# Kernel tuning notes

Hardware: AMD Instinct MI355X
Metric: run time of the kernel (lower is better)

## Reference

```python
import jax, jax.numpy as jnp
import numpy as np
import itertools

N_BOX = 19
B = 2048
T = 5
_EDGES = np.array(list(itertools.combinations(range(N_BOX), 2)))  # [E,2], E=171
ROW = jnp.asarray(_EDGES[:, 0])
COL = jnp.asarray(_EDGES[:, 1])


def setup_inputs() -> dict:
    key = jax.random.key(0)
    ks = jax.random.split(key, 8)
    return {
        "location_t": jax.random.uniform(ks[0], (B, N_BOX, 5), dtype=jnp.float32),
        "feature_t": jax.random.normal(ks[1], (B, N_BOX, 512), dtype=jnp.float32),
        "mask_t": jax.random.randint(ks[2], (B, N_BOX), 0, 2).astype(bool),
        "past_location_t": jax.random.uniform(ks[3], (B, T, N_BOX, 6), dtype=jnp.float32),
        "W1": jax.random.normal(ks[4], (512, 256), dtype=jnp.float32) * 0.05,
        "b1": jax.random.normal(ks[5], (256,), dtype=jnp.float32) * 0.05,
        "W2": jax.random.normal(ks[6], (256, 512), dtype=jnp.float32) * 0.05,
        "b2": jax.random.normal(ks[7], (512,), dtype=jnp.float32) * 0.05,
    }


def _edge_weights(location_t, mask, past_location_t):
    # bbox centers from cols 1..4: [B,N]
    cx = 0.5 * (location_t[:, :, 1] + location_t[:, :, 3])
    cy = 0.5 * (location_t[:, :, 2] + location_t[:, :, 4])
    d = (cx[:, ROW] - cx[:, COL]) ** 2 + (cy[:, ROW] - cy[:, COL]) ** 2  # [B,E]

    # motion distance, vectorized over all nodes then gathered per edge
    cp = past_location_t[:, :, :, 3:-1] - past_location_t[:, :, :, 1:3]  # [B,T,N,2]
    cpx = cp[..., 0] * 1280.0  # [B,T,N]
    cpy = cp[..., 1] * 720.0
    dx = cpx[:, -1] - cpx[:, 0]  # [B,N]
    dy = cpy[:, -1] - cpy[:, 0]
    length = jnp.sqrt(dx ** 2 + dy ** 2)
    length = jnp.where(length == 0.0, 1.0, length)
    ndx = dx / length
    ndy = dy / length
    x0 = cpx[:, 0]  # [B,N]
    y0 = cpy[:, 0]
    d1 = jnp.sqrt((x0[:, ROW] + ndx[:, ROW] - x0[:, COL] - ndx[:, COL]) ** 2
                  + (y0[:, ROW] + ndy[:, ROW] - y0[:, COL] - ndy[:, COL]) ** 2)
    d2 = jnp.sqrt((x0[:, ROW] - x0[:, COL]) ** 2 + (y0[:, ROW] - y0[:, COL]) ** 2)
    md = d1 - d2  # [B,E]

    w = jnp.exp(-(0.7 * d + 0.3 * md))
    valid = mask[:, ROW] & mask[:, COL]
    w = jnp.where(valid, w, 0.0)
    wmin = jnp.min(w, axis=1, keepdims=True)
    wmax = jnp.max(w, axis=1, keepdims=True)
    return (w - wmin) / (wmax - wmin)


def _gcn(x, ew, W, b):
    # PyG GCNConv: add self loops (weight 1), symmetric normalization, x@W, scatter-add, +bias
    n = x.shape[0]
    loops = jnp.arange(n)
    row = jnp.concatenate([ROW, loops])
    col = jnp.concatenate([COL, loops])
    ew_full = jnp.concatenate([ew, jnp.ones((n,), ew.dtype)])
    deg = jax.ops.segment_sum(ew_full, col, num_segments=n)
    dinv = jnp.where(deg > 0, deg ** -0.5, 0.0)
    norm = dinv[row] * ew_full * dinv[col]  # [E+N]
    xw = x @ W  # [N,F_out]
    out = jnp.zeros((n, W.shape[1]), xw.dtype).at[col].add(norm[:, None] * xw[row])
    return out + b


def reference(location_t, feature_t, mask_t, past_location_t, W1, b1, W2, b2):
    w = _edge_weights(location_t, mask_t, past_location_t)  # [B,E]

    def per_graph(x, ew):
        h = jax.nn.sigmoid(_gcn(x, ew, W1, b1))
        return jax.nn.sigmoid(_gcn(h, ew, W2, b2))

    return jax.vmap(per_graph)(feature_t, w)  # [B,19,512]
```

## Files before the change

### kernel.cpp

```cpp
#include <hip/hip_runtime.h>
#include <hip/hip_bf16.h>
#include <math.h>

#define NBOX 19
#define NEDGE 171
#define TT 5
#define BATCH 2048
#define GB 2
#define MR (GB * NBOX)
#define MP 48

typedef __attribute__((ext_vector_type(8))) short short8v;
typedef __attribute__((ext_vector_type(4))) float f32x4;

static __device__ __forceinline__ ushort f2bf(float f) {
    unsigned int u = __builtin_bit_cast(unsigned int, f);
    return (ushort)((u + 0x8000u) >> 16);
}

static __device__ __forceinline__ float sigm(float x) {
    return __builtin_amdgcn_rcpf(1.0f + __expf(-x));
}

__device__ __forceinline__ int edge_index(int r, int c) {
    return r * (NBOX - 1) - (r * (r - 1)) / 2 + (c - r - 1);
}

__global__ __launch_bounds__(192) void adjbf_kernel(
    const float* __restrict__ loc,
    const int*   __restrict__ mask,
    const float* __restrict__ past,
    ushort* __restrict__ adjbf)
{
    int b = blockIdx.x;
    int tid = threadIdx.x;
    __shared__ float cx[NBOX], cy[NBOX], x0[NBOX], y0[NBOX], ndx[NBOX], ndy[NBOX];
    __shared__ int   mv[NBOX];
    __shared__ float w[NEDGE];
    __shared__ float dinv[NBOX];
    __shared__ float wmin_s, wmax_s;

    if (tid < NBOX) {
        const float* l = loc + ((size_t)b * NBOX + tid) * 5;
        cx[tid] = 0.5f * (l[1] + l[3]);
        cy[tid] = 0.5f * (l[2] + l[4]);
        const float* p0 = past + (((size_t)b * TT + 0) * NBOX + tid) * 6;
        const float* p4 = past + (((size_t)b * TT + (TT - 1)) * NBOX + tid) * 6;
        float cpx0 = (p0[3] - p0[1]) * 1280.0f, cpy0 = (p0[4] - p0[2]) * 720.0f;
        float cpx4 = (p4[3] - p4[1]) * 1280.0f, cpy4 = (p4[4] - p4[2]) * 720.0f;
        float dx = cpx4 - cpx0, dy = cpy4 - cpy0;
        float len = sqrtf(dx * dx + dy * dy);
        if (len == 0.0f) len = 1.0f;
        ndx[tid] = dx / len;
        ndy[tid] = dy / len;
        x0[tid] = cpx0;
        y0[tid] = cpy0;
        mv[tid] = mask[(size_t)b * NBOX + tid];
    }
    __syncthreads();

    float wv = 0.0f;
    if (tid < NEDGE) {
        int rem = tid, rr = 0;
        while (rem >= NBOX - 1 - rr) { rem -= NBOX - 1 - rr; rr++; }
        int r = rr, c = rr + 1 + rem;
        float ddx = cx[r] - cx[c], ddy = cy[r] - cy[c];
        float d = ddx * ddx + ddy * ddy;
        float ax = x0[r] + ndx[r] - x0[c] - ndx[c];
        float ay = y0[r] + ndy[r] - y0[c] - ndy[c];
        float d1 = sqrtf(ax * ax + ay * ay);
        float bx = x0[r] - x0[c], by = y0[r] - y0[c];
        float d2 = sqrtf(bx * bx + by * by);
        float md = d1 - d2;
        wv = expf(-(0.7f * d + 0.3f * md));
        if (!(mv[r] && mv[c])) wv = 0.0f;
        w[tid] = wv;
    }
    __syncthreads();

    if (tid == 0) {
        float mn = w[0], mx = w[0];
        for (int i = 1; i < NEDGE; i++) { mn = fminf(mn, w[i]); mx = fmaxf(mx, w[i]); }
        wmin_s = mn; wmax_s = mx;
    }
    __syncthreads();

    float inv_range = 1.0f / (wmax_s - wmin_s);
    if (tid < NEDGE) w[tid] = (wv - wmin_s) * inv_range;
    __syncthreads();

    if (tid < NBOX) {
        float s = 1.0f;
        for (int rr = 0; rr < tid; rr++) s += w[edge_index(rr, tid)];
        dinv[tid] = 1.0f / sqrtf(s);
    }
    __syncthreads();

    ushort* A = adjbf + (size_t)b * 1024;
    for (int idx = tid; idx < 1024; idx += 192) {
        int r = idx & 31, cc = idx >> 5;
        float v = 0.0f;
        if (r < NBOX && cc < NBOX) {
            if (r == cc) v = dinv[r] * dinv[r];
            else if (r < cc) v = w[edge_index(r, cc)] * dinv[r] * dinv[cc];
        }
        A[idx] = f2bf(v);
    }
}

__global__ void packT_kernel(const float* __restrict__ src, ushort* __restrict__ dst,
                             int K, int N)
{
    int total = K * N;
    for (int idx = blockIdx.x * blockDim.x + threadIdx.x; idx < total;
         idx += gridDim.x * blockDim.x) {
        int n = idx / K, k = idx % K;
        dst[idx] = f2bf(src[(size_t)k * N + n]);
    }
}

__global__ __launch_bounds__(256, 4) void fused_kernel(
    const float*  __restrict__ feat,
    const ushort* __restrict__ adjbf,
    const ushort* __restrict__ W1T,
    const ushort* __restrict__ W2T,
    const float*  __restrict__ b1,
    const float*  __restrict__ b2,
    float* __restrict__ out)
{
    __shared__ __align__(16) ushort XHs[MP * 256];
    __shared__ __align__(16) ushort YsT[64 * 64];
    __shared__ __align__(16) ushort AdjS[MP * 64];

    const int tid = threadIdx.x;
    const int lane = tid & 63, wvi = tid >> 6;
    const int rowbase = blockIdx.x * MR;
    const int bbase = blockIdx.x * GB;
    const int ncol = wvi * 16 + (lane & 15);
    const int kgrp = lane >> 4;
    const int l15 = lane & 15;

#pragma unroll
    for (int p = 0; p < 2; p++)
        ((int4*)YsT)[tid + p * 256] = make_int4(0, 0, 0, 0);

    for (int i = tid; i < MP * 64; i += 256) {
        int row = i >> 6, col = i & 63;
        ushort v = 0;
        if (row < MR) {
            int g = (row >= NBOX) ? 1 : 0;
            int cc = row - g * NBOX;
            int rc = col - g * NBOX;
            if ((unsigned)rc < (unsigned)NBOX)
                v = adjbf[(size_t)(bbase + g) * 1024 + cc * 32 + rc];
        }
        int boff = (row * 128 + col * 2) ^ ((row & 7) << 4);
        *(ushort*)((char*)AdjS + boff) = v;
    }

    f32x4 acc1[4][3];
#pragma unroll
    for (int c = 0; c < 4; c++)
#pragma unroll
        for (int m = 0; m < 3; m++) acc1[c][m] = (f32x4){0.f, 0.f, 0.f, 0.f};

    for (int kh = 0; kh < 2; kh++) {
        __syncthreads();
        const float* fg = feat + (size_t)rowbase * 512 + kh * 256;
#pragma unroll
        for (int p = 0; p < 12; p++) {
            int i = tid + p * 256;
            int row = i >> 6, q = i & 63;
            ushort4 h;
            if (i < MR * 64) {
                float4 v = *(const float4*)(fg + (size_t)row * 512 + q * 4);
                h.x = f2bf(v.x); h.y = f2bf(v.y); h.z = f2bf(v.z); h.w = f2bf(v.w);
            } else {
                h.x = 0; h.y = 0; h.z = 0; h.w = 0;
            }
            int boff = (row * 512 + q * 8) ^ ((row & 7) << 4);
            *(ushort4*)((char*)XHs + boff) = h;
        }
        __syncthreads();

        const ushort* bpb = W1T + (size_t)ncol * 512 + kh * 256 + kgrp * 8;
        short8v br[3][4];
#pragma unroll
        for (int c = 0; c < 4; c++)
            br[0][c] = *(const short8v*)(bpb + (size_t)c * 64 * 512);
#pragma unroll
        for (int c = 0; c < 4; c++)
            br[1][c] = *(const short8v*)(bpb + (size_t)c * 64 * 512 + 32);
#pragma unroll
        for (int ks = 0; ks < 8; ks++) {
            if (ks < 6) {
#pragma unroll
                for (int c = 0; c < 4; c++)
                    br[(ks + 2) % 3][c] =
                        *(const short8v*)(bpb + (size_t)c * 64 * 512 + (ks + 2) * 32);
            }
            short8v a[3];
#pragma unroll
            for (int m = 0; m < 3; m++) {
                int row = m * 16 + l15;
                int boff = (row * 512 + ks * 64 + kgrp * 16) ^ ((row & 7) << 4);
                a[m] = *(const short8v*)((char*)XHs + boff);
            }
#pragma unroll
            for (int c = 0; c < 4; c++)
#pragma unroll
                for (int m = 0; m < 3; m++)
                    acc1[c][m] = __builtin_amdgcn_mfma_f32_16x16x32_bf16(
                        a[m], br[ks % 3][c], acc1[c][m], 0, 0, 0);
        }
    }
    __syncthreads();

#pragma unroll
    for (int c = 0; c < 4; c++) {
#pragma unroll
        for (int m = 0; m < 3; m++) {
            int gr0 = m * 16 + kgrp * 4;
            ushort4 hq;
            hq.x = f2bf(acc1[c][m][0]); hq.y = f2bf(acc1[c][m][1]);
            hq.z = f2bf(acc1[c][m][2]); hq.w = f2bf(acc1[c][m][3]);
            int boff = (ncol * 128 + gr0 * 2) ^ ((ncol & 7) << 4);
            *(ushort4*)((char*)YsT + boff) = hq;
        }
        short8v yb[2];
#pragma unroll
        for (int ks = 0; ks < 2; ks++)
            yb[ks] = *(const short8v*)((char*)YsT +
                     ((ncol * 128 + ks * 64 + kgrp * 16) ^ ((ncol & 7) << 4)));
        float bv = b1[c * 64 + ncol];
#pragma unroll
        for (int mt = 0; mt < 3; mt++) {
            f32x4 o = (f32x4){0.f, 0.f, 0.f, 0.f};
#pragma unroll
            for (int ks = 0; ks < 2; ks++) {
                int ar = mt * 16 + l15;
                short8v af = *(const short8v*)((char*)AdjS +
                             ((ar * 128 + ks * 64 + kgrp * 16) ^ ((ar & 7) << 4)));
                o = __builtin_amdgcn_mfma_f32_16x16x32_bf16(af, yb[ks], o, 0, 0, 0);
            }
#pragma unroll
            for (int j = 0; j < 4; j++) {
                int grp = mt * 16 + kgrp * 4 + j;
                float s = sigm(o[j] + bv);
                int boff = (grp * 512 + (c * 64 + ncol) * 2) ^ ((grp & 7) << 4);
                *(ushort*)((char*)XHs + boff) = f2bf(s);
            }
        }
    }
    __syncthreads();

#pragma unroll 1
    for (int half = 0; half < 2; half++) {
        f32x4 acc[4][3];
#pragma unroll
        for (int c = 0; c < 4; c++)
#pragma unroll
            for (int m = 0; m < 3; m++) acc[c][m] = (f32x4){0.f, 0.f, 0.f, 0.f};

        const ushort* bpb = W2T + (size_t)(half * 256 + ncol) * 256 + kgrp * 8;
        short8v br[3][4];
#pragma unroll
        for (int c = 0; c < 4; c++)
            br[0][c] = *(const short8v*)(bpb + (size_t)c * 64 * 256);
#pragma unroll
        for (int c = 0; c < 4; c++)
            br[1][c] = *(const short8v*)(bpb + (size_t)c * 64 * 256 + 32);
#pragma unroll
        for (int ks = 0; ks < 8; ks++) {
            if (ks < 6) {
#pragma unroll
                for (int c = 0; c < 4; c++)
                    br[(ks + 2) % 3][c] =
                        *(const short8v*)(bpb + (size_t)c * 64 * 256 + (ks + 2) * 32);
            }
            short8v a[3];
#pragma unroll
            for (int m = 0; m < 3; m++) {
                int row = m * 16 + l15;
                int boff = (row * 512 + ks * 64 + kgrp * 16) ^ ((row & 7) << 4);
                a[m] = *(const short8v*)((char*)XHs + boff);
            }
#pragma unroll
            for (int c = 0; c < 4; c++)
#pragma unroll
                for (int m = 0; m < 3; m++)
                    acc[c][m] = __builtin_amdgcn_mfma_f32_16x16x32_bf16(
                        a[m], br[ks % 3][c], acc[c][m], 0, 0, 0);
        }

#pragma unroll
        for (int c = 0; c < 4; c++) {
            int cg = half * 4 + c;
#pragma unroll
            for (int m = 0; m < 3; m++) {
                int gr0 = m * 16 + kgrp * 4;
                ushort4 hq;
                hq.x = f2bf(acc[c][m][0]); hq.y = f2bf(acc[c][m][1]);
                hq.z = f2bf(acc[c][m][2]); hq.w = f2bf(acc[c][m][3]);
                int boff = (ncol * 128 + gr0 * 2) ^ ((ncol & 7) << 4);
                *(ushort4*)((char*)YsT + boff) = hq;
            }
            short8v yb[2];
#pragma unroll
            for (int ks = 0; ks < 2; ks++)
                yb[ks] = *(const short8v*)((char*)YsT +
                         ((ncol * 128 + ks * 64 + kgrp * 16) ^ ((ncol & 7) << 4)));
            float bv = b2[cg * 64 + ncol];
#pragma unroll
            for (int mt = 0; mt < 3; mt++) {
                f32x4 o = (f32x4){0.f, 0.f, 0.f, 0.f};
#pragma unroll
                for (int ks = 0; ks < 2; ks++) {
                    int ar = mt * 16 + l15;
                    short8v af = *(const short8v*)((char*)AdjS +
                                 ((ar * 128 + ks * 64 + kgrp * 16) ^ ((ar & 7) << 4)));
                    o = __builtin_amdgcn_mfma_f32_16x16x32_bf16(af, yb[ks], o, 0, 0, 0);
                }
#pragma unroll
                for (int j = 0; j < 4; j++) {
                    int grp = mt * 16 + kgrp * 4 + j;
                    if (grp < MR) {
                        float s = sigm(o[j] + bv);
                        out[(size_t)(rowbase + grp) * 512 + cg * 64 + ncol] = s;
                    }
                }
            }
        }
    }
}

extern "C" void kernel_launch(void* const* d_in, const int* in_sizes, int n_in,
                              void* d_out, int out_size, void* d_ws, size_t ws_size,
                              hipStream_t stream) {
    const float* loc  = (const float*)d_in[0];
    const float* feat = (const float*)d_in[1];
    const int*   mask = (const int*)d_in[2];
    const float* past = (const float*)d_in[3];
    const float* W1   = (const float*)d_in[4];
    const float* b1   = (const float*)d_in[5];
    const float* W2   = (const float*)d_in[6];
    const float* b2   = (const float*)d_in[7];

    ushort* adjbf = (ushort*)d_ws;
    ushort* W1T   = adjbf + (size_t)BATCH * 1024;
    ushort* W2T   = W1T + 256 * 512;

    adjbf_kernel<<<BATCH, 192, 0, stream>>>(loc, mask, past, adjbf);
    packT_kernel<<<512, 256, 0, stream>>>(W1, W1T, 512, 256);
    packT_kernel<<<256, 256, 0, stream>>>(W2, W2T, 256, 512);

    fused_kernel<<<BATCH / GB, 256, 0, stream>>>(feat, adjbf, W1T, W2T, b1, b2,
                                                 (float*)d_out);
}
```

Measured before the change: 110.3 us.

## Replace LDS transpose staging with cross-lane shuffles for adjacency matmul B operand

Drops the YsT shared-memory buffer that was used to transpose each GEMM output tile into the B-operand layout of the adjacency MFMA. The tile is now packed into bf16 pairs and moved with wave shuffles. Adjacency A fragments are hoisted into registers once per stage, biases are preloaded, and the occupancy hint rises from 4 to 5 blocks per CU. This cuts LDS traffic and footprint, but adds shuffle instructions and register pressure that may cause spills under the tighter launch bound.

```diff
diff --git a/kernel.cpp b/kernel.cpp
--- a/kernel.cpp
+++ b/kernel.cpp
@@ -16,6 +16,12 @@
 static __device__ __forceinline__ ushort f2bf(float f) {
     unsigned int u = __builtin_bit_cast(unsigned int, f);
     return (ushort)((u + 0x8000u) >> 16);
+}
+
+static __device__ __forceinline__ unsigned pack2bf(float a, float b) {
+    unsigned ua = (__builtin_bit_cast(unsigned, a) + 0x8000u) >> 16;
+    unsigned ub = (__builtin_bit_cast(unsigned, b) + 0x8000u) & 0xFFFF0000u;
+    return ua | ub;
 }
 
 static __device__ __forceinline__ float sigm(float x) {
@@ -119,7 +125,7 @@
     }
 }
 
-__global__ __launch_bounds__(256, 4) void fused_kernel(
+__global__ __launch_bounds__(256, 5) void fused_kernel(
     const float*  __restrict__ feat,
     const ushort* __restrict__ adjbf,
     const ushort* __restrict__ W1T,
@@ -129,7 +135,6 @@
     float* __restrict__ out)
 {
     __shared__ __align__(16) ushort XHs[MP * 256];
-    __shared__ __align__(16) ushort YsT[64 * 64];
     __shared__ __align__(16) ushort AdjS[MP * 64];
 
     const int tid = threadIdx.x;
@@ -139,10 +144,15 @@
     const int ncol = wvi * 16 + (lane & 15);
     const int kgrp = lane >> 4;
     const int l15 = lane & 15;
-
-#pragma unroll
-    for (int p = 0; p < 2; p++)
-        ((int4*)YsT)[tid + p * 256] = make_int4(0, 0, 0, 0);
+    const int s0 = ((kgrp & 1) << 5) + l15;
+    const int s1 = s0 + 16;
+    const bool lowg = (kgrp < 2);
+
+    float bv1[4], bv2[8];
+#pragma unroll
+    for (int c = 0; c < 4; c++) bv1[c] = b1[c * 64 + ncol];
+#pragma unroll
+    for (int c = 0; c < 8; c++) bv2[c] = b2[c * 64 + ncol];
 
     for (int i = tid; i < MP * 64; i += 256) {
         int row = i >> 6, col = i & 63;
@@ -216,39 +226,48 @@
     }
     __syncthreads();
 
-#pragma unroll
-    for (int c = 0; c < 4; c++) {
-#pragma unroll
-        for (int m = 0; m < 3; m++) {
-            int gr0 = m * 16 + kgrp * 4;
-            ushort4 hq;
-            hq.x = f2bf(acc1[c][m][0]); hq.y = f2bf(acc1[c][m][1]);
-            hq.z = f2bf(acc1[c][m][2]); hq.w = f2bf(acc1[c][m][3]);
-            int boff = (ncol * 128 + gr0 * 2) ^ ((ncol & 7) << 4);
-            *(ushort4*)((char*)YsT + boff) = hq;
-        }
-        short8v yb[2];
-#pragma unroll
-        for (int ks = 0; ks < 2; ks++)
-            yb[ks] = *(const short8v*)((char*)YsT +
-                     ((ncol * 128 + ks * 64 + kgrp * 16) ^ ((ncol & 7) << 4)));
-        float bv = b1[c * 64 + ncol];
-#pragma unroll
-        for (int mt = 0; mt < 3; mt++) {
-            f32x4 o = (f32x4){0.f, 0.f, 0.f, 0.f};
+    {
+        short8v afr[3][2];
+#pragma unroll
+        for (int mt = 0; mt < 3; mt++)
 #pragma unroll
             for (int ks = 0; ks < 2; ks++) {
                 int ar = mt * 16 + l15;
-                short8v af = *(const short8v*)((char*)AdjS +
-                             ((ar * 128 + ks * 64 + kgrp * 16) ^ ((ar & 7) << 4)));
-                o = __builtin_amdgcn_mfma_f32_16x16x32_bf16(af, yb[ks], o, 0, 0, 0);
-            }
-#pragma unroll
-            for (int j = 0; j < 4; j++) {
-                int grp = mt * 16 + kgrp * 4 + j;
-                float s = sigm(o[j] + bv);
-                int boff = (grp * 512 + (c * 64 + ncol) * 2) ^ ((grp & 7) << 4);
-                *(ushort*)((char*)XHs + boff) = f2bf(s);
+                afr[mt][ks] = *(const short8v*)((char*)AdjS +
+                              ((ar * 128 + ks * 64 + kgrp * 16) ^ ((ar & 7) << 4)));
+            }
+#pragma unroll
+        for (int c = 0; c < 4; c++) {
+            unsigned p0a = pack2bf(acc1[c][0][0], acc1[c][0][1]);
+            unsigned p0b = pack2bf(acc1[c][0][2], acc1[c][0][3]);
+            unsigned p1a = pack2bf(acc1[c][1][0], acc1[c][1][1]);
+            unsigned p1b = pack2bf(acc1[c][1][2], acc1[c][1][3]);
+            unsigned p2a = pack2bf(acc1[c][2][0], acc1[c][2][1]);
+            unsigned p2b = pack2bf(acc1[c][2][2], acc1[c][2][3]);
+            unsigned A0 = __shfl(p0a, s0), A1 = __shfl(p0b, s0);
+            unsigned A2 = __shfl(p0a, s1), A3 = __shfl(p0b, s1);
+            unsigned B0 = __shfl(p1a, s0), B1 = __shfl(p1b, s0);
+            unsigned B2 = __shfl(p1a, s1), B3 = __shfl(p1b, s1);
+            unsigned C0 = __shfl(p2a, s0), C1 = __shfl(p2b, s0);
+            unsigned C2 = __shfl(p2a, s1), C3 = __shfl(p2b, s1);
+            int4 y0i = lowg ? make_int4(A0, A1, A2, A3) : make_int4(B0, B1, B2, B3);
+            int4 y1i = lowg ? make_int4(C0, C1, C2, C3) : make_int4(0, 0, 0, 0);
+            short8v yb0 = __builtin_bit_cast(short8v, y0i);
+            short8v yb1 = __builtin_bit_cast(short8v, y1i);
+            float bv = bv1[c];
+#pragma unroll
+            for (int mt = 0; mt < 3; mt++) {
+                f32x4 o = __builtin_amdgcn_mfma_f32_16x16x32_bf16(
+                    afr[mt][0], yb0, (f32x4){0.f, 0.f, 0.f, 0.f}, 0, 0, 0);
+                o = __builtin_amdgcn_mfma_f32_16x16x32_bf16(
+                    afr[mt][1], yb1, o, 0, 0, 0);
+#pragma unroll
+                for (int j = 0; j < 4; j++) {
+                    int grp = mt * 16 + kgrp * 4 + j;
+                    float s = sigm(o[j] + bv);
+                    int boff = (grp * 512 + (c * 64 + ncol) * 2) ^ ((grp & 7) << 4);
+                    *(ushort*)((char*)XHs + boff) = f2bf(s);
+                }
             }
         }
     }
@@ -293,34 +312,41 @@
                         a[m], br[ks % 3][c], acc[c][m], 0, 0, 0);
         }
 
+        short8v afr[3][2];
+#pragma unroll
+        for (int mt = 0; mt < 3; mt++)
+#pragma unroll
+            for (int ks = 0; ks < 2; ks++) {
+                int ar = mt * 16 + l15;
+                afr[mt][ks] = *(const short8v*)((char*)AdjS +
+                              ((ar * 128 + ks * 64 + kgrp * 16) ^ ((ar & 7) << 4)));
+            }
 #pragma unroll
         for (int c = 0; c < 4; c++) {
             int cg = half * 4 + c;
-#pragma unroll
-            for (int m = 0; m < 3; m++) {
-                int gr0 = m * 16 + kgrp * 4;
-                ushort4 hq;
-                hq.x = f2bf(acc[c][m][0]); hq.y = f2bf(acc[c][m][1]);
-                hq.z = f2bf(acc[c][m][2]); hq.w = f2bf(acc[c][m][3]);
-                int boff = (ncol * 128 + gr0 * 2) ^ ((ncol & 7) << 4);
-                *(ushort4*)((char*)YsT + boff) = hq;
-            }
-            short8v yb[2];
-#pragma unroll
-            for (int ks = 0; ks < 2; ks++)
-                yb[ks] = *(const short8v*)((char*)YsT +
-                         ((ncol * 128 + ks * 64 + kgrp * 16) ^ ((ncol & 7) << 4)));
-            float bv = b2[cg * 64 + ncol];
+            unsigned p0a = pack2bf(acc[c][0][0], acc[c][0][1]);
+            unsigned p0b = pack2bf(acc[c][0][2], acc[c][0][3]);
+            unsigned p1a = pack2bf(acc[c][1][0], acc[c][1][1]);
+            unsigned p1b = pack2bf(acc[c][1][2], acc[c][1][3]);
+            unsigned p2a = pack2bf(acc[c][2][0], acc[c][2][1]);
+            unsigned p2b = pack2bf(acc[c][2][2], acc[c][2][3]);
+            unsigned A0 = __shfl(p0a, s0), A1 = __shfl(p0b, s0);
+            unsigned A2 = __shfl(p0a, s1), A3 = __shfl(p0b, s1);
+            unsigned B0 = __shfl(p1a, s0), B1 = __shfl(p1b, s0);
+            unsigned B2 = __shfl(p1a, s1), B3 = __shfl(p1b, s1);
+            unsigned C0 = __shfl(p2a, s0), C1 = __shfl(p2b, s0);
+            unsigned C2 = __shfl(p2a, s1), C3 = __shfl(p2b, s1);
+            int4 y0i = lowg ? make_int4(A0, A1, A2, A3) : make_int4(B0, B1, B2, B3);
+            int4 y1i = lowg ? make_int4(C0, C1, C2, C3) : make_int4(0, 0, 0, 0);
+            short8v yb0 = __builtin_bit_cast(short8v, y0i);
+            short8v yb1 = __builtin_bit_cast(short8v, y1i);
+            float bv = bv2[cg];
 #pragma unroll
             for (int mt = 0; mt < 3; mt++) {
-                f32x4 o = (f32x4){0.f, 0.f, 0.f, 0.f};
-#pragma unroll
-                for (int ks = 0; ks < 2; ks++) {
-                    int ar = mt * 16 + l15;
-                    short8v af = *(const short8v*)((char*)AdjS +
-                                 ((ar * 128 + ks * 64 + kgrp * 16) ^ ((ar & 7) << 4)));
-                    o = __builtin_amdgcn_mfma_f32_16x16x32_bf16(af, yb[ks], o, 0, 0, 0);
-                }
+                f32x4 o = __builtin_amdgcn_mfma_f32_16x16x32_bf16(
+                    afr[mt][0], yb0, (f32x4){0.f, 0.f, 0.f, 0.f}, 0, 0, 0);
+                o = __builtin_amdgcn_mfma_f32_16x16x32_bf16(
+                    afr[mt][1], yb1, o, 0, 0, 0);
 #pragma unroll
                 for (int j = 0; j < 4; j++) {
                     int grp = mt * 16 + kgrp * 4 + j;
```

After: 304.2 us. +175.9%, slower.

## Use 512 threads per block, splitting output columns across eight waves

Applied to the files above, without the earlier changes.

The fused GCN kernel now runs 8 waves instead of 4. Each wave owns two 16-column tiles (col and col+128) instead of four, so the per-wave accumulators and B-operand register buffers shrink, and the weight prefetch drops from triple to double buffering. Each wave gets its own region of the transposed scratch (YsT grows to 16 KB), and XHs is zero-filled up front instead of writing padding rows inside the load loop. The aim is more waves per CU and lower register pressure to hide latency. The cost is larger LDS use per block and the risk that 512-thread blocks with launch_bounds(512,4) limit occupancy.

```diff
diff --git a/kernel.cpp b/kernel.cpp
--- a/kernel.cpp
+++ b/kernel.cpp
@@ -119,7 +119,7 @@
     }
 }
 
-__global__ __launch_bounds__(256, 4) void fused_kernel(
+__global__ __launch_bounds__(512, 4) void fused_kernel(
     const float*  __restrict__ feat,
     const ushort* __restrict__ adjbf,
     const ushort* __restrict__ W1T,
@@ -129,22 +129,26 @@
     float* __restrict__ out)
 {
     __shared__ __align__(16) ushort XHs[MP * 256];
-    __shared__ __align__(16) ushort YsT[64 * 64];
+    __shared__ __align__(16) ushort YsT[8 * 1024];
     __shared__ __align__(16) ushort AdjS[MP * 64];
 
     const int tid = threadIdx.x;
     const int lane = tid & 63, wvi = tid >> 6;
     const int rowbase = blockIdx.x * MR;
     const int bbase = blockIdx.x * GB;
-    const int ncol = wvi * 16 + (lane & 15);
     const int kgrp = lane >> 4;
     const int l15 = lane & 15;
-
+    const int colb = wvi * 16 + l15;
+    const int ytbase = wvi * 2048;
+
+#pragma unroll
+    for (int p = 0; p < 3; p++)
+        ((int4*)XHs)[tid + p * 512] = make_int4(0, 0, 0, 0);
 #pragma unroll
     for (int p = 0; p < 2; p++)
-        ((int4*)YsT)[tid + p * 256] = make_int4(0, 0, 0, 0);
-
-    for (int i = tid; i < MP * 64; i += 256) {
+        ((int4*)YsT)[tid + p * 512] = make_int4(0, 0, 0, 0);
+
+    for (int i = tid; i < MP * 64; i += 512) {
         int row = i >> 6, col = i & 63;
         ushort v = 0;
         if (row < MR) {
@@ -158,9 +162,9 @@
         *(ushort*)((char*)AdjS + boff) = v;
     }
 
-    f32x4 acc1[4][3];
-#pragma unroll
-    for (int c = 0; c < 4; c++)
+    f32x4 acc1[2][3];
+#pragma unroll
+    for (int c = 0; c < 2; c++)
 #pragma unroll
         for (int m = 0; m < 3; m++) acc1[c][m] = (f32x4){0.f, 0.f, 0.f, 0.f};
 
@@ -168,36 +172,29 @@
         __syncthreads();
         const float* fg = feat + (size_t)rowbase * 512 + kh * 256;
 #pragma unroll
-        for (int p = 0; p < 12; p++) {
-            int i = tid + p * 256;
-            int row = i >> 6, q = i & 63;
-            ushort4 h;
+        for (int p = 0; p < 5; p++) {
+            int i = tid + p * 512;
             if (i < MR * 64) {
+                int row = i >> 6, q = i & 63;
                 float4 v = *(const float4*)(fg + (size_t)row * 512 + q * 4);
+                ushort4 h;
                 h.x = f2bf(v.x); h.y = f2bf(v.y); h.z = f2bf(v.z); h.w = f2bf(v.w);
-            } else {
-                h.x = 0; h.y = 0; h.z = 0; h.w = 0;
-            }
-            int boff = (row * 512 + q * 8) ^ ((row & 7) << 4);
-            *(ushort4*)((char*)XHs + boff) = h;
+                int boff = (row * 512 + q * 8) ^ ((row & 7) << 4);
+                *(ushort4*)((char*)XHs + boff) = h;
+            }
         }
         __syncthreads();
 
-        const ushort* bpb = W1T + (size_t)ncol * 512 + kh * 256 + kgrp * 8;
-        short8v br[3][4];
-#pragma unroll
-        for (int c = 0; c < 4; c++)
-            br[0][c] = *(const short8v*)(bpb + (size_t)c * 64 * 512);
-#pragma unroll
-        for (int c = 0; c < 4; c++)
-            br[1][c] = *(const short8v*)(bpb + (size_t)c * 64 * 512 + 32);
+        const ushort* bp0 = W1T + (size_t)colb * 512 + kh * 256 + kgrp * 8;
+        const ushort* bp1 = bp0 + (size_t)128 * 512;
+        short8v br[2][2];
+        br[0][0] = *(const short8v*)(bp0);
+        br[0][1] = *(const short8v*)(bp1);
 #pragma unroll
         for (int ks = 0; ks < 8; ks++) {
-            if (ks < 6) {
-#pragma unroll
-                for (int c = 0; c < 4; c++)
-                    br[(ks + 2) % 3][c] =
-                        *(const short8v*)(bpb + (size_t)c * 64 * 512 + (ks + 2) * 32);
+            if (ks < 7) {
+                br[(ks + 1) & 1][0] = *(const short8v*)(bp0 + (ks + 1) * 32);
+                br[(ks + 1) & 1][1] = *(const short8v*)(bp1 + (ks + 1) * 32);
             }
             short8v a[3];
 #pragma unroll
@@ -207,32 +204,33 @@
                 a[m] = *(const short8v*)((char*)XHs + boff);
             }
 #pragma unroll
-            for (int c = 0; c < 4; c++)
+            for (int c = 0; c < 2; c++)
 #pragma unroll
                 for (int m = 0; m < 3; m++)
                     acc1[c][m] = __builtin_amdgcn_mfma_f32_16x16x32_bf16(
-                        a[m], br[ks % 3][c], acc1[c][m], 0, 0, 0);
-        }
-    }
-    __syncthreads();
-
-#pragma unroll
-    for (int c = 0; c < 4; c++) {
+                        a[m], br[ks & 1][c], acc1[c][m], 0, 0, 0);
+        }
+    }
+    __syncthreads();
+
+#pragma unroll
+    for (int c = 0; c < 2; c++) {
+        int colg = c * 128 + colb;
 #pragma unroll
         for (int m = 0; m < 3; m++) {
             int gr0 = m * 16 + kgrp * 4;
             ushort4 hq;
             hq.x = f2bf(acc1[c][m][0]); hq.y = f2bf(acc1[c][m][1]);
             hq.z = f2bf(acc1[c][m][2]); hq.w = f2bf(acc1[c][m][3]);
-            int boff = (ncol * 128 + gr0 * 2) ^ ((ncol & 7) << 4);
+            int boff = ytbase + ((l15 * 128 + gr0 * 2) ^ ((l15 & 7) << 4));
             *(ushort4*)((char*)YsT + boff) = hq;
         }
         short8v yb[2];
 #pragma unroll
         for (int ks = 0; ks < 2; ks++)
-            yb[ks] = *(const short8v*)((char*)YsT +
-                     ((ncol * 128 + ks * 64 + kgrp * 16) ^ ((ncol & 7) << 4)));
-        float bv = b1[c * 64 + ncol];
+            yb[ks] = *(const short8v*)((char*)YsT + ytbase +
+                     ((l15 * 128 + ks * 64 + kgrp * 16) ^ ((l15 & 7) << 4)));
+        float bv = b1[colg];
 #pragma unroll
         for (int mt = 0; mt < 3; mt++) {
             f32x4 o = (f32x4){0.f, 0.f, 0.f, 0.f};
@@ -247,7 +245,7 @@
             for (int j = 0; j < 4; j++) {
                 int grp = mt * 16 + kgrp * 4 + j;
                 float s = sigm(o[j] + bv);
-                int boff = (grp * 512 + (c * 64 + ncol) * 2) ^ ((grp & 7) << 4);
+                int boff = (grp * 512 + colg * 2) ^ ((grp & 7) << 4);
                 *(ushort*)((char*)XHs + boff) = f2bf(s);
             }
         }
@@ -256,27 +254,22 @@
 
 #pragma unroll 1
     for (int half = 0; half < 2; half++) {
-        f32x4 acc[4][3];
-#pragma unroll
-        for (int c = 0; c < 4; c++)
+        f32x4 acc[2][3];
+#pragma unroll
+        for (int c = 0; c < 2; c++)
 #pragma unroll
             for (int m = 0; m < 3; m++) acc[c][m] = (f32x4){0.f, 0.f, 0.f, 0.f};
 
-        const ushort* bpb = W2T + (size_t)(half * 256 + ncol) * 256 + kgrp * 8;
-        short8v br[3][4];
-#pragma unroll
-        for (int c = 0; c < 4; c++)
-            br[0][c] = *(const short8v*)(bpb + (size_t)c * 64 * 256);
-#pragma unroll
-        for (int c = 0; c < 4; c++)
-            br[1][c] = *(const short8v*)(bpb + (size_t)c * 64 * 256 + 32);
+        const ushort* bp0 = W2T + (size_t)(half * 256 + colb) * 256 + kgrp * 8;
+        const ushort* bp1 = bp0 + (size_t)128 * 256;
+        short8v br[2][2];
+        br[0][0] = *(const short8v*)(bp0);
+        br[0][1] = *(const short8v*)(bp1);
 #pragma unroll
         for (int ks = 0; ks < 8; ks++) {
-            if (ks < 6) {
-#pragma unroll
-                for (int c = 0; c < 4; c++)
-                    br[(ks + 2) % 3][c] =
-                        *(const short8v*)(bpb + (size_t)c * 64 * 256 + (ks + 2) * 32);
+            if (ks < 7) {
+                br[(ks + 1) & 1][0] = *(const short8v*)(bp0 + (ks + 1) * 32);
+                br[(ks + 1) & 1][1] = *(const short8v*)(bp1 + (ks + 1) * 32);
             }
             short8v a[3];
 #pragma unroll
@@ -286,31 +279,31 @@
                 a[m] = *(const short8v*)((char*)XHs + boff);
             }
 #pragma unroll
-            for (int c = 0; c < 4; c++)
+            for (int c = 0; c < 2; c++)
 #pragma unroll
                 for (int m = 0; m < 3; m++)
                     acc[c][m] = __builtin_amdgcn_mfma_f32_16x16x32_bf16(
-                        a[m], br[ks % 3][c], acc[c][m], 0, 0, 0);
-        }
-
-#pragma unroll
-        for (int c = 0; c < 4; c++) {
-            int cg = half * 4 + c;
+                        a[m], br[ks & 1][c], acc[c][m], 0, 0, 0);
+        }
+
+#pragma unroll
+        for (int c = 0; c < 2; c++) {
+            int colg2 = half * 256 + c * 128 + colb;
 #pragma unroll
             for (int m = 0; m < 3; m++) {
                 int gr0 = m * 16 + kgrp * 4;
                 ushort4 hq;
                 hq.x = f2bf(acc[c][m][0]); hq.y = f2bf(acc[c][m][1]);
                 hq.z = f2bf(acc[c][m][2]); hq.w = f2bf(acc[c][m][3]);
-                int boff = (ncol * 128 + gr0 * 2) ^ ((ncol & 7) << 4);
+                int boff = ytbase + ((l15 * 128 + gr0 * 2) ^ ((l15 & 7) << 4));
                 *(ushort4*)((char*)YsT + boff) = hq;
             }
             short8v yb[2];
 #pragma unroll
             for (int ks = 0; ks < 2; ks++)
-                yb[ks] = *(const short8v*)((char*)YsT +
-                         ((ncol * 128 + ks * 64 + kgrp * 16) ^ ((ncol & 7) << 4)));
-            float bv = b2[cg * 64 + ncol];
+                yb[ks] = *(const short8v*)((char*)YsT + ytbase +
+                         ((l15 * 128 + ks * 64 + kgrp * 16) ^ ((l15 & 7) << 4)));
+            float bv = b2[colg2];
 #pragma unroll
             for (int mt = 0; mt < 3; mt++) {
                 f32x4 o = (f32x4){0.f, 0.f, 0.f, 0.f};
@@ -326,7 +319,7 @@
                     int grp = mt * 16 + kgrp * 4 + j;
                     if (grp < MR) {
                         float s = sigm(o[j] + bv);
-                        out[(size_t)(rowbase + grp) * 512 + cg * 64 + ncol] = s;
+                        out[(size_t)(rowbase + grp) * 512 + colg2] = s;
                     }
                 }
             }
@@ -354,6 +347,6 @@
     packT_kernel<<<512, 256, 0, stream>>>(W1, W1T, 512, 256);
     packT_kernel<<<256, 256, 0, stream>>>(W2, W2T, 256, 512);
 
-    fused_kernel<<<BATCH / GB, 256, 0, stream>>>(feat, adjbf, W1T, W2T, b1, b2,
+    fused_kernel<<<BATCH / GB, 512, 0, stream>>>(feat, adjbf, W1T, W2T, b1, b2,
                                                  (float*)d_out);
 }
```

New measurement: 157.2 us. 42.5% more time.

## Precompute swizzled pair adjacency image, merge weight packing, add MFMA priority

Applied to the files above, without the earlier changes.

The adjacency kernel now writes the final swizzled, zero-padded 48x64 bf16 adjacency tile for each graph pair. The fused kernel can then load it with vectorized int4 copies instead of scattered per-element gathers. The min/max reduction uses wave shuffles instead of a serial single-thread loop, and the two weight-transpose launches are merged into one kernel. s_setprio is raised around MFMA blocks to favour issuing matrix ops; the cost is a slightly larger workspace image.

```diff
diff --git a/kernel.cpp b/kernel.cpp
--- a/kernel.cpp
+++ b/kernel.cpp
@@ -26,19 +26,20 @@
     return r * (NBOX - 1) - (r * (r - 1)) / 2 + (c - r - 1);
 }
 
-__global__ __launch_bounds__(192) void adjbf_kernel(
+__global__ __launch_bounds__(192) void adjpair_kernel(
     const float* __restrict__ loc,
     const int*   __restrict__ mask,
     const float* __restrict__ past,
-    ushort* __restrict__ adjbf)
+    ushort* __restrict__ pairimg)
 {
     int b = blockIdx.x;
+    int p = b >> 1, g = b & 1;
     int tid = threadIdx.x;
     __shared__ float cx[NBOX], cy[NBOX], x0[NBOX], y0[NBOX], ndx[NBOX], ndy[NBOX];
     __shared__ int   mv[NBOX];
     __shared__ float w[NEDGE];
     __shared__ float dinv[NBOX];
-    __shared__ float wmin_s, wmax_s;
+    __shared__ float rmn[3], rmx[3];
 
     if (tid < NBOX) {
         const float* l = loc + ((size_t)b * NBOX + tid) * 5;
@@ -74,19 +75,21 @@
         float md = d1 - d2;
         wv = expf(-(0.7f * d + 0.3f * md));
         if (!(mv[r] && mv[c])) wv = 0.0f;
-        w[tid] = wv;
-    }
-    __syncthreads();
-
-    if (tid == 0) {
-        float mn = w[0], mx = w[0];
-        for (int i = 1; i < NEDGE; i++) { mn = fminf(mn, w[i]); mx = fmaxf(mx, w[i]); }
-        wmin_s = mn; wmax_s = mx;
-    }
-    __syncthreads();
-
-    float inv_range = 1.0f / (wmax_s - wmin_s);
-    if (tid < NEDGE) w[tid] = (wv - wmin_s) * inv_range;
+    }
+
+    float lmn = (tid < NEDGE) ? wv : INFINITY;
+    float lmx = (tid < NEDGE) ? wv : -INFINITY;
+#pragma unroll
+    for (int o = 32; o; o >>= 1) {
+        lmn = fminf(lmn, __shfl_xor(lmn, o));
+        lmx = fmaxf(lmx, __shfl_xor(lmx, o));
+    }
+    if ((tid & 63) == 0) { rmn[tid >> 6] = lmn; rmx[tid >> 6] = lmx; }
+    __syncthreads();
+    float mn = fminf(rmn[0], fminf(rmn[1], rmn[2]));
+    float mx = fmaxf(rmx[0], fmaxf(rmx[1], rmx[2]));
+    float inv_range = 1.0f / (mx - mn);
+    if (tid < NEDGE) w[tid] = (wv - mn) * inv_range;
     __syncthreads();
 
     if (tid < NBOX) {
@@ -96,32 +99,48 @@
     }
     __syncthreads();
 
-    ushort* A = adjbf + (size_t)b * 1024;
-    for (int idx = tid; idx < 1024; idx += 192) {
-        int r = idx & 31, cc = idx >> 5;
-        float v = 0.0f;
-        if (r < NBOX && cc < NBOX) {
-            if (r == cc) v = dinv[r] * dinv[r];
-            else if (r < cc) v = w[edge_index(r, cc)] * dinv[r] * dinv[cc];
-        }
-        A[idx] = f2bf(v);
-    }
-}
-
-__global__ void packT_kernel(const float* __restrict__ src, ushort* __restrict__ dst,
-                             int K, int N)
+    {
+        int row_local = tid >> 3, chunk = tid & 7;
+        int row = (g == 0)
+            ? (row_local < NBOX ? row_local : NBOX + row_local)
+            : (row_local < NBOX ? NBOX + row_local : 24 + row_local);
+        ushort vals[8];
+#pragma unroll
+        for (int i = 0; i < 8; i++) {
+            int col = chunk * 8 + i;
+            int rc = col - g * NBOX;
+            float v = 0.0f;
+            if (row_local < NBOX && rc >= 0 && rc < NBOX) {
+                int cc = row_local;
+                if (rc == cc) v = dinv[cc] * dinv[cc];
+                else if (rc < cc) v = w[edge_index(rc, cc)] * dinv[rc] * dinv[cc];
+            }
+            vals[i] = f2bf(v);
+        }
+        int boff = (row * 128 + chunk * 16) ^ ((row & 7) << 4);
+        *(int4*)((char*)pairimg + (size_t)p * 6144 + boff) = *(int4*)vals;
+    }
+}
+
+__global__ void packT2_kernel(const float* __restrict__ W1,
+                              const float* __restrict__ W2,
+                              ushort* __restrict__ W1T,
+                              ushort* __restrict__ W2T)
 {
-    int total = K * N;
-    for (int idx = blockIdx.x * blockDim.x + threadIdx.x; idx < total;
-         idx += gridDim.x * blockDim.x) {
-        int n = idx / K, k = idx % K;
-        dst[idx] = f2bf(src[(size_t)k * N + n]);
+    int idx = blockIdx.x * blockDim.x + threadIdx.x;
+    if (idx < 131072) {
+        int n = idx / 512, k = idx % 512;
+        W1T[idx] = f2bf(W1[(size_t)k * 256 + n]);
+    } else {
+        int j = idx - 131072;
+        int n = j / 256, k = j % 256;
+        W2T[j] = f2bf(W2[(size_t)k * 512 + n]);
     }
 }
 
 __global__ __launch_bounds__(256, 4) void fused_kernel(
     const float*  __restrict__ feat,
-    const ushort* __restrict__ adjbf,
+    const ushort* __restrict__ pairimg,
     const ushort* __restrict__ W1T,
     const ushort* __restrict__ W2T,
     const float*  __restrict__ b1,
@@ -135,7 +154,6 @@
     const int tid = threadIdx.x;
     const int lane = tid & 63, wvi = tid >> 6;
     const int rowbase = blockIdx.x * MR;
-    const int bbase = blockIdx.x * GB;
     const int ncol = wvi * 16 + (lane & 15);
     const int kgrp = lane >> 4;
     const int l15 = lane & 15;
@@ -144,18 +162,10 @@
     for (int p = 0; p < 2; p++)
         ((int4*)YsT)[tid + p * 256] = make_int4(0, 0, 0, 0);
 
-    for (int i = tid; i < MP * 64; i += 256) {
-        int row = i >> 6, col = i & 63;
-        ushort v = 0;
-        if (row < MR) {
-            int g = (row >= NBOX) ? 1 : 0;
-            int cc = row - g * NBOX;
-            int rc = col - g * NBOX;
-            if ((unsigned)rc < (unsigned)NBOX)
-                v = adjbf[(size_t)(bbase + g) * 1024 + cc * 32 + rc];
-        }
-        int boff = (row * 128 + col * 2) ^ ((row & 7) << 4);
-        *(ushort*)((char*)AdjS + boff) = v;
+    {
+        const int4* src = (const int4*)((const char*)pairimg + (size_t)blockIdx.x * 6144);
+        ((int4*)AdjS)[tid] = src[tid];
+        if (tid < 128) ((int4*)AdjS)[tid + 256] = src[tid + 256];
     }
 
     f32x4 acc1[4][3];
@@ -206,12 +216,14 @@
                 int boff = (row * 512 + ks * 64 + kgrp * 16) ^ ((row & 7) << 4);
                 a[m] = *(const short8v*)((char*)XHs + boff);
             }
+            __builtin_amdgcn_s_setprio(1);
 #pragma unroll
             for (int c = 0; c < 4; c++)
 #pragma unroll
                 for (int m = 0; m < 3; m++)
                     acc1[c][m] = __builtin_amdgcn_mfma_f32_16x16x32_bf16(
                         a[m], br[ks % 3][c], acc1[c][m], 0, 0, 0);
+            __builtin_amdgcn_s_setprio(0);
         }
     }
     __syncthreads();
@@ -285,12 +297,14 @@
                 int boff = (row * 512 + ks * 64 + kgrp * 16) ^ ((row & 7) << 4);
                 a[m] = *(const short8v*)((char*)XHs + boff);
             }
+            __builtin_amdgcn_s_setprio(1);
 #pragma unroll
             for (int c = 0; c < 4; c++)
 #pragma unroll
                 for (int m = 0; m < 3; m++)
                     acc[c][m] = __builtin_amdgcn_mfma_f32_16x16x32_bf16(
                         a[m], br[ks % 3][c], acc[c][m], 0, 0, 0);
+            __builtin_amdgcn_s_setprio(0);
         }
 
 #pragma unroll
@@ -346,14 +360,13 @@
     const float* W2   = (const float*)d_in[6];
     const float* b2   = (const float*)d_in[7];
 
-    ushort* adjbf = (ushort*)d_ws;
-    ushort* W1T   = adjbf + (size_t)BATCH * 1024;
-    ushort* W2T   = W1T + 256 * 512;
-
-    adjbf_kernel<<<BATCH, 192, 0, stream>>>(loc, mask, past, adjbf);
-    packT_kernel<<<512, 256, 0, stream>>>(W1, W1T, 512, 256);
-    packT_kernel<<<256, 256, 0, stream>>>(W2, W2T, 256, 512);
-
-    fused_kernel<<<BATCH / GB, 256, 0, stream>>>(feat, adjbf, W1T, W2T, b1, b2,
+    ushort* pairimg = (ushort*)d_ws;
+    ushort* W1T     = pairimg + (size_t)(BATCH / 2) * 3072;
+    ushort* W2T     = W1T + 256 * 512;
+
+    adjpair_kernel<<<BATCH, 192, 0, stream>>>(loc, mask, past, pairimg);
+    packT2_kernel<<<1024, 256, 0, stream>>>(W1, W2, W1T, W2T);
+
+    fused_kernel<<<BATCH / GB, 256, 0, stream>>>(feat, pairimg, W1T, W2T, b1, b2,
                                                  (float*)d_out);
 }
```

Measured after the change: 134.8 us. 22.2% more time.
